# Optimization experiments

Hardware: AMD Instinct MI355X
Metric: run time of the kernel (lower is better)

The kernel has to match this reference:

```python
import jax, jax.numpy as jnp
import numpy as np

NUM_HEADS = 16


def setup_inputs() -> dict:
    key = jax.random.key(0)
    ks = jax.random.split(key, 11)
    B, S, D = 2, 8192, 1024
    scale = 1.0 / np.sqrt(D).astype(np.float32)
    return {
        "v": jax.random.normal(ks[0], (B, S, D), jnp.float32),
        "k": jax.random.normal(ks[1], (B, S, D), jnp.float32),
        "q": jax.random.normal(ks[2], (B, S, D), jnp.float32),
        "Wq": jax.random.normal(ks[3], (D, D), jnp.float32) * scale,
        "bq": jnp.zeros((D,), jnp.float32),
        "Wk": jax.random.normal(ks[4], (D, D), jnp.float32) * scale,
        "bk": jnp.zeros((D,), jnp.float32),
        "Wv": jax.random.normal(ks[5], (D, D), jnp.float32) * scale,
        "bv": jnp.zeros((D,), jnp.float32),
        "Wo": jax.random.normal(ks[6], (D, D), jnp.float32) * scale,
        "bo": jnp.zeros((D,), jnp.float32),
    }


def _mha(v, k, q, Wq, bq, Wk, bk, Wv, bv, Wo, bo):
    H = NUM_HEADS
    d_model = Wq.shape[1]
    depth = d_model // H
    # linear projections, split into heads: [B, S, H, depth]
    qh = (q @ Wq + bq).reshape(*q.shape[:-1], H, depth)
    kh = (k @ Wk + bk).reshape(*k.shape[:-1], H, depth)
    vh = (v @ Wv + bv).reshape(*v.shape[:-1], H, depth)
    # scaled dot-product attention. The original uses a chunked online-softmax
    # (memory-efficient attention, arXiv:2112.05682) which computes the exact
    # same softmax(QK^T/sqrt(d))V; we express it directly.
    scale = 1.0 / jnp.sqrt(jnp.asarray(depth, qh.dtype))
    logits = jnp.einsum('bqhd,bkhd->bhqk', qh * scale, kh,
                        precision=jax.lax.Precision.HIGHEST)
    attn = jax.nn.softmax(logits, axis=-1)
    out = jnp.einsum('bhqk,bkhd->bqhd', attn, vh,
                     precision=jax.lax.Precision.HIGHEST)
    out = out.reshape(*out.shape[:-2], d_model)
    return out @ Wo + bo


def reference(v, k, q, Wq, bq, Wk, bk, Wv, bv, Wo, bo):
    return _mha(v, k, q, Wq, bq, Wk, bk, Wv, bv, Wo, bo)
```

## Files before the change

### kernel.cpp

```cpp
#include <hip/hip_runtime.h>
#include <math.h>
#include <stdint.h>

#define H 16
#define Dm 1024
#define DH2 64
#define SLEN 8192
#define BATCH 2
#define KVBLK 64

#define WAIT_VM0 0x0F70

#if __has_builtin(__builtin_amdgcn_exp2f)
#define NEXP2(x) __builtin_amdgcn_exp2f(x)
#else
#define NEXP2(x) __builtin_exp2f(x)
#endif

typedef __attribute__((ext_vector_type(8))) short bf16x8;
typedef __attribute__((ext_vector_type(2))) float f32x2;
typedef __attribute__((ext_vector_type(4))) float f32x4;
typedef __attribute__((ext_vector_type(16))) float f32x16;
typedef __attribute__((ext_vector_type(4))) short short4v;
typedef __attribute__((ext_vector_type(4))) unsigned int uint4v;
typedef __attribute__((ext_vector_type(2))) int int2v;

#define MFMA16(a,b,c) __builtin_amdgcn_mfma_f32_16x16x32_bf16(a,b,c,0,0,0)
#define MFMA32(a,b,c) __builtin_amdgcn_mfma_f32_32x32x16_bf16(a,b,c,0,0,0)

static __device__ __forceinline__ short f2b(float f){
  unsigned u = __builtin_bit_cast(unsigned, f);
  u += 0x7fffu + ((u >> 16) & 1u);
  return (short)(u >> 16);
}

static __device__ __forceinline__ void gload16(const void* g, void* l){
  __builtin_amdgcn_global_load_lds((const __attribute__((address_space(1))) void*)g,
                                   (__attribute__((address_space(3))) void*)l, 16, 0, 0);
}

static __device__ __forceinline__ bf16x8 mkfrag_pk(const f32x2* v){
  unsigned p0, p1, p2, p3;
  asm("v_cvt_pk_bf16_f32 %0, %1, %2" : "=v"(p0) : "v"(v[0].x), "v"(v[0].y));
  asm("v_cvt_pk_bf16_f32 %0, %1, %2" : "=v"(p1) : "v"(v[1].x), "v"(v[1].y));
  asm("v_cvt_pk_bf16_f32 %0, %1, %2" : "=v"(p2) : "v"(v[2].x), "v"(v[2].y));
  asm("v_cvt_pk_bf16_f32 %0, %1, %2" : "=v"(p3) : "v"(v[3].x), "v"(v[3].y));
  uint4v u = (uint4v){p0, p1, p2, p3};
  return __builtin_bit_cast(bf16x8, u);
}

struct S8 { f32x2 v[8]; };

__global__ __launch_bounds__(256) void transpose_w_kernel(
    const float* __restrict__ Wq, const float* __restrict__ Wk,
    const float* __restrict__ Wv, const float* __restrict__ Wo,
    short* __restrict__ WqT, short* __restrict__ WkT,
    short* __restrict__ WvT, short* __restrict__ WoT)
{
  const float* W; short* WT;
  switch (blockIdx.z){
    case 0: W = Wq; WT = WqT; break;
    case 1: W = Wk; WT = WkT; break;
    case 2: W = Wv; WT = WvT; break;
    default: W = Wo; WT = WoT; break;
  }
  __shared__ float t[32][33];
  int tx = threadIdx.x & 31, ty = threadIdx.x >> 5;
  int x0 = blockIdx.x * 32, y0 = blockIdx.y * 32;
  for (int j = 0; j < 4; ++j){
    int r = ty + j * 8;
    t[r][tx] = W[(size_t)(y0 + r) * Dm + x0 + tx];
  }
  __syncthreads();
  for (int j = 0; j < 4; ++j){
    int r = ty + j * 8;
    WT[(size_t)(x0 + r) * Dm + y0 + tx] = f2b(t[tx][r]);
  }
}

__global__ __launch_bounds__(256) void proj_kernel(
    const float* __restrict__ Aq, const float* __restrict__ Ak, const float* __restrict__ Av,
    const short* __restrict__ WqT, const short* __restrict__ WkT, const short* __restrict__ WvT,
    const float* __restrict__ bq, const float* __restrict__ bk, const float* __restrict__ bv,
    short* __restrict__ Qh, short* __restrict__ Kh, short* __restrict__ VhT)
{
  const float* A; const short* WT; const float* bias;
  int z = blockIdx.z;
  if (z == 0){ A = Aq; WT = WqT; bias = bq; }
  else if (z == 1){ A = Ak; WT = WkT; bias = bk; }
  else { A = Av; WT = WvT; bias = bv; }

  __shared__ __align__(16) char smem[34816];
  short (*As)[64] = (short(*)[64])smem;
  short* Bs = (short*)(smem + 16384);

  int tid = threadIdx.x;
  int lane = tid & 63, w = tid >> 6;
  int l15 = lane & 15, lh = lane >> 4;
  int wm = w >> 1, wn = w & 1;
  int m0 = blockIdx.x * 128, n0 = blockIdx.y * 128;

  f32x4 acc[4][4];
  for (int i = 0; i < 4; ++i)
    for (int j = 0; j < 4; ++j)
      acc[i][j] = (f32x4){0.f, 0.f, 0.f, 0.f};

  for (int ko = 0; ko < 16; ++ko){
    for (int j = 0; j < 8; ++j){
      int idx = j * 256 + tid;
      int r = idx >> 4, c4 = idx & 15;
      float4 a = *(const float4*)(A + (size_t)(m0 + r) * Dm + ko * 64 + c4 * 4);
      short4v p; p[0] = f2b(a.x); p[1] = f2b(a.y); p[2] = f2b(a.z); p[3] = f2b(a.w);
      *(short4v*)&As[r][c4 * 4] = p;
    }
    for (int j = 0; j < 4; ++j){
      int c = w * 4 + j;
      int row = c * 8 + (lane >> 3), seg = lane & 7;
      gload16(WT + (size_t)(n0 + row) * Dm + ko * 64 + seg * 8, Bs + c * 512);
    }
    __builtin_amdgcn_s_waitcnt(WAIT_VM0);
    __syncthreads();
    for (int kk = 0; kk < 2; ++kk){
      bf16x8 af[4];
      for (int i = 0; i < 4; ++i)
        af[i] = *(const bf16x8*)&As[wm * 64 + i * 16 + l15][kk * 32 + lh * 8];
      for (int jj = 0; jj < 4; ++jj){
        bf16x8 bfv = *(const bf16x8*)(Bs + (size_t)(wn * 64 + jj * 16 + l15) * 64 + kk * 32 + lh * 8);
        for (int i = 0; i < 4; ++i)
          acc[i][jj] = MFMA16(af[i], bfv, acc[i][jj]);
      }
    }
    __syncthreads();
  }

  if (z < 2){
    short* out = (z == 0) ? Qh : Kh;
    float scale = (z == 0) ? 0.18033688011112042f : 1.0f;
    for (int jj = 0; jj < 4; ++jj){
      int col = n0 + wn * 64 + jj * 16 + l15;
      float bb = bias[col];
      int h = col >> 6, d = col & 63;
      for (int i = 0; i < 4; ++i)
        for (int r = 0; r < 4; ++r){
          int row = m0 + wm * 64 + i * 16 + lh * 4 + r;
          int b = row >> 13, s = row & 8191;
          out[(((size_t)b * H + h) * SLEN + s) * DH2 + d] = f2b((acc[i][jj][r] + bb) * scale);
        }
    }
  } else {
    short (*Ct)[136] = (short(*)[136])smem;
    for (int jj = 0; jj < 4; ++jj){
      int colL = wn * 64 + jj * 16 + l15;
      float bb = bias[n0 + colL];
      for (int i = 0; i < 4; ++i)
        for (int r = 0; r < 4; ++r){
          int rowL = wm * 64 + i * 16 + lh * 4 + r;
          Ct[colL][rowL] = f2b(acc[i][jj][r] + bb);
        }
    }
    __syncthreads();
    int b = m0 >> 13, s0 = m0 & 8191;
    for (int p = 0; p < 8; ++p){
      int rowC = p * 16 + (tid >> 4), seg = tid & 15;
      int4 vv = *(const int4*)&Ct[rowC][seg * 8];
      int ngl = n0 + rowC, h = ngl >> 6, d = ngl & 63;
      size_t base = (((size_t)b * H + h) * DH2 + d) * SLEN + s0;
      int sA = seg * 8;
      int b16 = sA & ~15;
      int half = (sA >> 3) & 1;
      int2v lo = (int2v){ ((int*)&vv)[0], ((int*)&vv)[1] };
      int2v hi2 = (int2v){ ((int*)&vv)[2], ((int*)&vv)[3] };
      *(int2v*)&VhT[base + b16 + half * 4]     = lo;
      *(int2v*)&VhT[base + b16 + 8 + half * 4] = hi2;
    }
  }
}

__global__ __launch_bounds__(512, 2) void attn_kernel(
    const short* __restrict__ Qh, const short* __restrict__ Kh,
    const short* __restrict__ VhT, short* __restrict__ attn_out)
{
  __shared__ __align__(16) short Ktile[2][4096];
  __shared__ __align__(16) short Vtile[2][4096];
  __shared__ float redbuf[8][32];

  const int tid = threadIdx.x;
  const int lane = tid & 63;
  const int w = tid >> 6;
  const int l31 = lane & 31;
  const int hi = lane >> 5;
  const int bh = blockIdx.y;
  const int q0 = blockIdx.x * 256 + w * 32;

  const short* Qbase = Qh + ((size_t)bh * SLEN + q0) * DH2;
  const short* Kbase = Kh + (size_t)bh * SLEN * DH2;
  const short* Vbase = VhT + (size_t)bh * DH2 * SLEN;

  bf16x8 qf[4];
#pragma unroll
  for (int ds = 0; ds < 4; ++ds)
    qf[ds] = *(const bf16x8*)(Qbase + (size_t)l31 * DH2 + ds * 16 + hi * 8);

  f32x16 Oa0, Oa1;
#pragma unroll
  for (int i = 0; i < 16; ++i){ Oa0[i] = 0.f; Oa1[i] = 0.f; }
  float l_run = 0.f;

  int koff[4];
#pragma unroll
  for (int ds = 0; ds < 4; ++ds)
    koff[ds] = l31 * 64 + (((ds * 2 + hi) ^ (l31 & 7)) * 8);
  int voff[2][4];
#pragma unroll
  for (int n = 0; n < 2; ++n)
#pragma unroll
    for (int st = 0; st < 4; ++st)
      voff[n][st] = (n * 32 + l31) * 64 + (((st * 2 + hi) ^ (l31 & 7)) * 8);

  const short* spK = Kbase + (size_t)(tid >> 3) * DH2 + (((tid & 7) ^ ((tid >> 3) & 7)) * 8);
  const short* spV = Vbase + (size_t)(tid >> 3) * SLEN + (((tid & 7) ^ ((tid >> 3) & 7)) * 8);
  short* dK0 = Ktile[0] + tid * 8; short* dK1 = Ktile[1] + tid * 8;
  short* dV0 = Vtile[0] + tid * 8; short* dV1 = Vtile[1] + tid * 8;

  gload16(spK, dK0); gload16(spV, dV0);
  spK += (size_t)KVBLK * DH2; spV += KVBLK;

  const int NT = SLEN / KVBLK;

  auto tile = [&](const short* Kt, const short* Vt, bool do_stage,
                  short* dK, short* dV){
    __builtin_amdgcn_s_waitcnt(WAIT_VM0);
    __syncthreads();
    if (do_stage){
      gload16(spK, dK);
      gload16(spV, dV);
      spK += (size_t)KVBLK * DH2; spV += KVBLK;
    }

    f32x16 sa0, sa1;
#pragma unroll
    for (int i = 0; i < 16; ++i){ sa0[i] = 0.f; sa1[i] = 0.f; }
#pragma unroll
    for (int ds = 0; ds < 4; ++ds){
      bf16x8 kf0 = *(const bf16x8*)(Kt + koff[ds]);
      bf16x8 kf1 = *(const bf16x8*)(Kt + koff[ds] + 32 * 64);
      sa0 = MFMA32(kf0, qf[ds], sa0);
      sa1 = MFMA32(kf1, qf[ds], sa1);
    }

    S8 t0 = __builtin_bit_cast(S8, sa0);
    S8 t1 = __builtin_bit_cast(S8, sa1);
#pragma unroll
    for (int i = 0; i < 8; ++i){
      t0.v[i].x = NEXP2(t0.v[i].x);
      t0.v[i].y = NEXP2(t0.v[i].y);
      t1.v[i].x = NEXP2(t1.v[i].x);
      t1.v[i].y = NEXP2(t1.v[i].y);
    }

    f32x2 s0 = ((t0.v[0] + t0.v[1]) + (t0.v[2] + t0.v[3])) +
               ((t0.v[4] + t0.v[5]) + (t0.v[6] + t0.v[7]));
    f32x2 s1 = ((t1.v[0] + t1.v[1]) + (t1.v[2] + t1.v[3])) +
               ((t1.v[4] + t1.v[5]) + (t1.v[6] + t1.v[7]));
    f32x2 st = s0 + s1;
    l_run += st.x + st.y;

    bf16x8 pa0 = mkfrag_pk(&t0.v[0]);
    bf16x8 pa1 = mkfrag_pk(&t0.v[4]);
    bf16x8 pa2 = mkfrag_pk(&t1.v[0]);
    bf16x8 pa3 = mkfrag_pk(&t1.v[4]);

    bf16x8 vb;
    vb = *(const bf16x8*)(Vt + voff[0][0]); Oa0 = MFMA32(pa0, vb, Oa0);
    vb = *(const bf16x8*)(Vt + voff[1][0]); Oa1 = MFMA32(pa0, vb, Oa1);
    vb = *(const bf16x8*)(Vt + voff[0][1]); Oa0 = MFMA32(pa1, vb, Oa0);
    vb = *(const bf16x8*)(Vt + voff[1][1]); Oa1 = MFMA32(pa1, vb, Oa1);
    vb = *(const bf16x8*)(Vt + voff[0][2]); Oa0 = MFMA32(pa2, vb, Oa0);
    vb = *(const bf16x8*)(Vt + voff[1][2]); Oa1 = MFMA32(pa2, vb, Oa1);
    vb = *(const bf16x8*)(Vt + voff[0][3]); Oa0 = MFMA32(pa3, vb, Oa0);
    vb = *(const bf16x8*)(Vt + voff[1][3]); Oa1 = MFMA32(pa3, vb, Oa1);
  };

  for (int kt = 0; kt < NT; kt += 2){
    tile(Ktile[0], Vtile[0], true,          dK1, dV1);
    tile(Ktile[1], Vtile[1], kt + 2 < NT,   dK0, dV0);
  }

  float l_tot = l_run + __shfl_xor(l_run, 32);
  float inv = 1.0f / l_tot;
  redbuf[w][l31] = inv;
  int b = bh >> 4, h = bh & 15;
#pragma unroll
  for (int j = 0; j < 4; ++j){
    f32x4 iv = *(const f32x4*)&redbuf[w][j * 8 + hi * 4];
#pragma unroll
    for (int i = 0; i < 4; ++i){
      int qi = j * 8 + hi * 4 + i;
      size_t rowoff = ((size_t)b * SLEN + q0 + qi) * Dm + h * 64;
      attn_out[rowoff + l31]      = f2b(Oa0[j * 4 + i] * iv[i]);
      attn_out[rowoff + 32 + l31] = f2b(Oa1[j * 4 + i] * iv[i]);
    }
  }
}

__global__ __launch_bounds__(256) void oproj_kernel(
    const short* __restrict__ Aattn, const short* __restrict__ WoT,
    const float* __restrict__ bo, float* __restrict__ out)
{
  __shared__ __align__(16) char smem[32768];
  short* As = (short*)smem;
  short* Bs = (short*)(smem + 16384);

  int tid = threadIdx.x;
  int lane = tid & 63, w = tid >> 6;
  int l15 = lane & 15, lh = lane >> 4;
  int wm = w >> 1, wn = w & 1;
  int m0 = blockIdx.x * 128, n0 = blockIdx.y * 128;

  f32x4 acc[4][4];
  for (int i = 0; i < 4; ++i)
    for (int j = 0; j < 4; ++j)
      acc[i][j] = (f32x4){0.f, 0.f, 0.f, 0.f};

  for (int ko = 0; ko < 16; ++ko){
    for (int j = 0; j < 4; ++j){
      int c = w * 4 + j;
      int row = c * 8 + (lane >> 3), seg = lane & 7;
      gload16(Aattn + (size_t)(m0 + row) * Dm + ko * 64 + seg * 8, As + c * 512);
      gload16(WoT   + (size_t)(n0 + row) * Dm + ko * 64 + seg * 8, Bs + c * 512);
    }
    __builtin_amdgcn_s_waitcnt(WAIT_VM0);
    __syncthreads();
    for (int kk = 0; kk < 2; ++kk){
      bf16x8 af[4];
      for (int i = 0; i < 4; ++i)
        af[i] = *(const bf16x8*)(As + (size_t)(wm * 64 + i * 16 + l15) * 64 + kk * 32 + lh * 8);
      for (int jj = 0; jj < 4; ++jj){
        bf16x8 bfv = *(const bf16x8*)(Bs + (size_t)(wn * 64 + jj * 16 + l15) * 64 + kk * 32 + lh * 8);
        for (int i = 0; i < 4; ++i)
          acc[i][jj] = MFMA16(af[i], bfv, acc[i][jj]);
      }
    }
    __syncthreads();
  }
  for (int jj = 0; jj < 4; ++jj){
    int col = n0 + wn * 64 + jj * 16 + l15;
    float bb = bo[col];
    for (int i = 0; i < 4; ++i)
      for (int r = 0; r < 4; ++r){
        int row = m0 + wm * 64 + i * 16 + lh * 4 + r;
        out[(size_t)row * Dm + col] = acc[i][jj][r] + bb;
      }
  }
}

extern "C" void kernel_launch(void* const* d_in, const int* in_sizes, int n_in,
                              void* d_out, int out_size, void* d_ws, size_t ws_size,
                              hipStream_t stream)
{
  const float* v  = (const float*)d_in[0];
  const float* k  = (const float*)d_in[1];
  const float* q  = (const float*)d_in[2];
  const float* Wq = (const float*)d_in[3];
  const float* bq = (const float*)d_in[4];
  const float* Wk = (const float*)d_in[5];
  const float* bk = (const float*)d_in[6];
  const float* Wv = (const float*)d_in[7];
  const float* bv = (const float*)d_in[8];
  const float* Wo = (const float*)d_in[9];
  const float* bo = (const float*)d_in[10];
  float* out = (float*)d_out;

  char* ws = (char*)d_ws;
  const size_t MB = 1u << 20;
  short* WqT = (short*)(ws + 0 * MB);
  short* WkT = (short*)(ws + 2 * MB);
  short* WvT = (short*)(ws + 4 * MB);
  short* WoT = (short*)(ws + 6 * MB);
  short* Qh  = (short*)(ws + 8 * MB);
  short* Kh  = (short*)(ws + 40 * MB);
  short* VhT = (short*)(ws + 72 * MB);
  short* Ao  = (short*)(ws + 104 * MB);

  transpose_w_kernel<<<dim3(32, 32, 4), 256, 0, stream>>>(Wq, Wk, Wv, Wo, WqT, WkT, WvT, WoT);
  proj_kernel<<<dim3(128, 8, 3), 256, 0, stream>>>(q, k, v, WqT, WkT, WvT, bq, bk, bv, Qh, Kh, VhT);
  attn_kernel<<<dim3(32, 32), 512, 0, stream>>>(Qh, Kh, VhT, Ao);
  oproj_kernel<<<dim3(128, 8), 256, 0, stream>>>(Ao, WoT, bo, out);
}
```

Before: 829.3 us.

## Precast activations to bf16 and double attention KV tile size

Adds a separate kernel that casts the q/k/v activations to bf16 once, so each projection block can stage A tiles with direct global-to-LDS loads instead of re-reading fp32 and converting per n-block. Separately, the attention KV block grows from 64 to 128 keys, with each tile processed as two 64-key halves, halving the number of barrier/stage iterations. The precast path costs extra workspace and an extra full pass over the inputs, and the larger LDS footprint may cut attention occupancy.

```diff
diff --git a/kernel.cpp b/kernel.cpp
--- a/kernel.cpp
+++ b/kernel.cpp
@@ -7,7 +7,7 @@
 #define DH2 64
 #define SLEN 8192
 #define BATCH 2
-#define KVBLK 64
+#define KVBLK 128
 
 #define WAIT_VM0 0x0F70
 
@@ -51,6 +51,30 @@
 
 struct S8 { f32x2 v[8]; };
 
+__global__ __launch_bounds__(256) void cast_a_kernel(
+    const float* __restrict__ q, const float* __restrict__ k, const float* __restrict__ v,
+    short* __restrict__ Aq, short* __restrict__ Ak, short* __restrict__ Av)
+{
+  const float* src; short* dst;
+  switch (blockIdx.y){
+    case 0: src = q; dst = Aq; break;
+    case 1: src = k; dst = Ak; break;
+    default: src = v; dst = Av; break;
+  }
+  const size_t n = (size_t)BATCH * SLEN * Dm;
+  size_t i0 = ((size_t)blockIdx.x * 256 + threadIdx.x) * 8;
+  size_t stride = (size_t)gridDim.x * 256 * 8;
+  for (size_t i = i0; i < n; i += stride){
+    float4 a = *(const float4*)(src + i);
+    float4 b = *(const float4*)(src + i + 4);
+    short4v p, r;
+    p[0] = f2b(a.x); p[1] = f2b(a.y); p[2] = f2b(a.z); p[3] = f2b(a.w);
+    r[0] = f2b(b.x); r[1] = f2b(b.y); r[2] = f2b(b.z); r[3] = f2b(b.w);
+    *(short4v*)(dst + i) = p;
+    *(short4v*)(dst + i + 4) = r;
+  }
+}
+
 __global__ __launch_bounds__(256) void transpose_w_kernel(
     const float* __restrict__ Wq, const float* __restrict__ Wk,
     const float* __restrict__ Wv, const float* __restrict__ Wo,
@@ -78,20 +102,23 @@
   }
 }
 
+template<bool PRECAST>
 __global__ __launch_bounds__(256) void proj_kernel(
-    const float* __restrict__ Aq, const float* __restrict__ Ak, const float* __restrict__ Av,
+    const float* __restrict__ Afq, const float* __restrict__ Afk, const float* __restrict__ Afv,
+    const short* __restrict__ Abq, const short* __restrict__ Abk, const short* __restrict__ Abv,
     const short* __restrict__ WqT, const short* __restrict__ WkT, const short* __restrict__ WvT,
     const float* __restrict__ bq, const float* __restrict__ bk, const float* __restrict__ bv,
     short* __restrict__ Qh, short* __restrict__ Kh, short* __restrict__ VhT)
 {
-  const float* A; const short* WT; const float* bias;
+  const float* Af; const short* Ab; const short* WT; const float* bias;
   int z = blockIdx.z;
-  if (z == 0){ A = Aq; WT = WqT; bias = bq; }
-  else if (z == 1){ A = Ak; WT = WkT; bias = bk; }
-  else { A = Av; WT = WvT; bias = bv; }
+  if (z == 0){ Af = Afq; Ab = Abq; WT = WqT; bias = bq; }
+  else if (z == 1){ Af = Afk; Ab = Abk; WT = WkT; bias = bk; }
+  else { Af = Afv; Ab = Abv; WT = WvT; bias = bv; }
 
   __shared__ __align__(16) char smem[34816];
   short (*As)[64] = (short(*)[64])smem;
+  short* Asl = (short*)smem;
   short* Bs = (short*)(smem + 16384);
 
   int tid = threadIdx.x;
@@ -106,12 +133,20 @@
       acc[i][j] = (f32x4){0.f, 0.f, 0.f, 0.f};
 
   for (int ko = 0; ko < 16; ++ko){
-    for (int j = 0; j < 8; ++j){
-      int idx = j * 256 + tid;
-      int r = idx >> 4, c4 = idx & 15;
-      float4 a = *(const float4*)(A + (size_t)(m0 + r) * Dm + ko * 64 + c4 * 4);
-      short4v p; p[0] = f2b(a.x); p[1] = f2b(a.y); p[2] = f2b(a.z); p[3] = f2b(a.w);
-      *(short4v*)&As[r][c4 * 4] = p;
+    if (PRECAST){
+      for (int j = 0; j < 4; ++j){
+        int c = w * 4 + j;
+        int row = c * 8 + (lane >> 3), seg = lane & 7;
+        gload16(Ab + (size_t)(m0 + row) * Dm + ko * 64 + seg * 8, Asl + c * 512);
+      }
+    } else {
+      for (int j = 0; j < 8; ++j){
+        int idx = j * 256 + tid;
+        int r = idx >> 4, c4 = idx & 15;
+        float4 a = *(const float4*)(Af + (size_t)(m0 + r) * Dm + ko * 64 + c4 * 4);
+        short4v p; p[0] = f2b(a.x); p[1] = f2b(a.y); p[2] = f2b(a.z); p[3] = f2b(a.w);
+        *(short4v*)&As[r][c4 * 4] = p;
+      }
     }
     for (int j = 0; j < 4; ++j){
       int c = w * 4 + j;
@@ -149,6 +184,7 @@
     }
   } else {
     short (*Ct)[136] = (short(*)[136])smem;
+    __syncthreads();
     for (int jj = 0; jj < 4; ++jj){
       int colL = wn * 64 + jj * 16 + l15;
       float bb = bias[n0 + colL];
@@ -180,8 +216,8 @@
     const short* __restrict__ Qh, const short* __restrict__ Kh,
     const short* __restrict__ VhT, short* __restrict__ attn_out)
 {
-  __shared__ __align__(16) short Ktile[2][4096];
-  __shared__ __align__(16) short Vtile[2][4096];
+  __shared__ __align__(16) short Ktile[2][8192];
+  __shared__ __align__(16) short Vtile[2][8192];
   __shared__ float redbuf[8][32];
 
   const int tid = threadIdx.x;
@@ -201,9 +237,9 @@
   for (int ds = 0; ds < 4; ++ds)
     qf[ds] = *(const bf16x8*)(Qbase + (size_t)l31 * DH2 + ds * 16 + hi * 8);
 
-  f32x16 Oa0, Oa1;
-#pragma unroll
-  for (int i = 0; i < 16; ++i){ Oa0[i] = 0.f; Oa1[i] = 0.f; }
+  f32x16 Oa0, Oa1, Zacc;
+#pragma unroll
+  for (int i = 0; i < 16; ++i){ Oa0[i] = 0.f; Oa1[i] = 0.f; Zacc[i] = 0.f; }
   float l_run = 0.f;
 
   int koff[4];
@@ -215,14 +251,16 @@
   for (int n = 0; n < 2; ++n)
 #pragma unroll
     for (int st = 0; st < 4; ++st)
-      voff[n][st] = (n * 32 + l31) * 64 + (((st * 2 + hi) ^ (l31 & 7)) * 8);
+      voff[n][st] = (n * 32 + l31) * 128 + (((st * 2 + hi) ^ (l31 & 7)) * 8);
 
   const short* spK = Kbase + (size_t)(tid >> 3) * DH2 + (((tid & 7) ^ ((tid >> 3) & 7)) * 8);
-  const short* spV = Vbase + (size_t)(tid >> 3) * SLEN + (((tid & 7) ^ ((tid >> 3) & 7)) * 8);
+  const int vkc = tid & 15, vh = vkc >> 3, vc8 = vkc & 7, vd = tid >> 4;
+  const short* spV = Vbase + (size_t)vd * SLEN + vh * 64 + ((vc8 ^ (vd & 7)) * 8);
   short* dK0 = Ktile[0] + tid * 8; short* dK1 = Ktile[1] + tid * 8;
   short* dV0 = Vtile[0] + tid * 8; short* dV1 = Vtile[1] + tid * 8;
 
-  gload16(spK, dK0); gload16(spV, dV0);
+  gload16(spK, dK0); gload16(spK + 64 * DH2, dK0 + 4096);
+  gload16(spV, dV0); gload16(spV + (size_t)32 * SLEN, dV0 + 4096);
   spK += (size_t)KVBLK * DH2; spV += KVBLK;
 
   const int NT = SLEN / KVBLK;
@@ -232,58 +270,65 @@
     __builtin_amdgcn_s_waitcnt(WAIT_VM0);
     __syncthreads();
     if (do_stage){
-      gload16(spK, dK);
-      gload16(spV, dV);
+      gload16(spK, dK); gload16(spK + 64 * DH2, dK + 4096);
+      gload16(spV, dV); gload16(spV + (size_t)32 * SLEN, dV + 4096);
       spK += (size_t)KVBLK * DH2; spV += KVBLK;
     }
 
-    f32x16 sa0, sa1;
-#pragma unroll
-    for (int i = 0; i < 16; ++i){ sa0[i] = 0.f; sa1[i] = 0.f; }
-#pragma unroll
-    for (int ds = 0; ds < 4; ++ds){
-      bf16x8 kf0 = *(const bf16x8*)(Kt + koff[ds]);
-      bf16x8 kf1 = *(const bf16x8*)(Kt + koff[ds] + 32 * 64);
-      sa0 = MFMA32(kf0, qf[ds], sa0);
-      sa1 = MFMA32(kf1, qf[ds], sa1);
-    }
-
-    S8 t0 = __builtin_bit_cast(S8, sa0);
-    S8 t1 = __builtin_bit_cast(S8, sa1);
-#pragma unroll
-    for (int i = 0; i < 8; ++i){
-      t0.v[i].x = NEXP2(t0.v[i].x);
-      t0.v[i].y = NEXP2(t0.v[i].y);
-      t1.v[i].x = NEXP2(t1.v[i].x);
-      t1.v[i].y = NEXP2(t1.v[i].y);
-    }
-
-    f32x2 s0 = ((t0.v[0] + t0.v[1]) + (t0.v[2] + t0.v[3])) +
-               ((t0.v[4] + t0.v[5]) + (t0.v[6] + t0.v[7]));
-    f32x2 s1 = ((t1.v[0] + t1.v[1]) + (t1.v[2] + t1.v[3])) +
-               ((t1.v[4] + t1.v[5]) + (t1.v[6] + t1.v[7]));
-    f32x2 st = s0 + s1;
-    l_run += st.x + st.y;
-
-    bf16x8 pa0 = mkfrag_pk(&t0.v[0]);
-    bf16x8 pa1 = mkfrag_pk(&t0.v[4]);
-    bf16x8 pa2 = mkfrag_pk(&t1.v[0]);
-    bf16x8 pa3 = mkfrag_pk(&t1.v[4]);
-
-    bf16x8 vb;
-    vb = *(const bf16x8*)(Vt + voff[0][0]); Oa0 = MFMA32(pa0, vb, Oa0);
-    vb = *(const bf16x8*)(Vt + voff[1][0]); Oa1 = MFMA32(pa0, vb, Oa1);
-    vb = *(const bf16x8*)(Vt + voff[0][1]); Oa0 = MFMA32(pa1, vb, Oa0);
-    vb = *(const bf16x8*)(Vt + voff[1][1]); Oa1 = MFMA32(pa1, vb, Oa1);
-    vb = *(const bf16x8*)(Vt + voff[0][2]); Oa0 = MFMA32(pa2, vb, Oa0);
-    vb = *(const bf16x8*)(Vt + voff[1][2]); Oa1 = MFMA32(pa2, vb, Oa1);
-    vb = *(const bf16x8*)(Vt + voff[0][3]); Oa0 = MFMA32(pa3, vb, Oa0);
-    vb = *(const bf16x8*)(Vt + voff[1][3]); Oa1 = MFMA32(pa3, vb, Oa1);
+#pragma unroll
+    for (int half = 0; half < 2; ++half){
+      const short* Kh_ = Kt + half * 4096;
+      const short* Vh_ = Vt + half * 64;
+
+      bf16x8 kf0 = *(const bf16x8*)(Kh_ + koff[0]);
+      bf16x8 kf1 = *(const bf16x8*)(Kh_ + koff[0] + 2048);
+      f32x16 sa0 = MFMA32(kf0, qf[0], Zacc);
+      f32x16 sa1 = MFMA32(kf1, qf[0], Zacc);
+#pragma unroll
+      for (int ds = 1; ds < 4; ++ds){
+        kf0 = *(const bf16x8*)(Kh_ + koff[ds]);
+        kf1 = *(const bf16x8*)(Kh_ + koff[ds] + 2048);
+        sa0 = MFMA32(kf0, qf[ds], sa0);
+        sa1 = MFMA32(kf1, qf[ds], sa1);
+      }
+
+      S8 t0 = __builtin_bit_cast(S8, sa0);
+      S8 t1 = __builtin_bit_cast(S8, sa1);
+#pragma unroll
+      for (int i = 0; i < 8; ++i){
+        t0.v[i].x = NEXP2(t0.v[i].x);
+        t0.v[i].y = NEXP2(t0.v[i].y);
+        t1.v[i].x = NEXP2(t1.v[i].x);
+        t1.v[i].y = NEXP2(t1.v[i].y);
+      }
+
+      f32x2 s0 = ((t0.v[0] + t0.v[1]) + (t0.v[2] + t0.v[3])) +
+                 ((t0.v[4] + t0.v[5]) + (t0.v[6] + t0.v[7]));
+      f32x2 s1 = ((t1.v[0] + t1.v[1]) + (t1.v[2] + t1.v[3])) +
+                 ((t1.v[4] + t1.v[5]) + (t1.v[6] + t1.v[7]));
+      f32x2 st = s0 + s1;
+      l_run += st.x + st.y;
+
+      bf16x8 pa0 = mkfrag_pk(&t0.v[0]);
+      bf16x8 pa1 = mkfrag_pk(&t0.v[4]);
+      bf16x8 pa2 = mkfrag_pk(&t1.v[0]);
+      bf16x8 pa3 = mkfrag_pk(&t1.v[4]);
+
+      bf16x8 vb;
+      vb = *(const bf16x8*)(Vh_ + voff[0][0]); Oa0 = MFMA32(pa0, vb, Oa0);
+      vb = *(const bf16x8*)(Vh_ + voff[1][0]); Oa1 = MFMA32(pa0, vb, Oa1);
+      vb = *(const bf16x8*)(Vh_ + voff[0][1]); Oa0 = MFMA32(pa1, vb, Oa0);
+      vb = *(const bf16x8*)(Vh_ + voff[1][1]); Oa1 = MFMA32(pa1, vb, Oa1);
+      vb = *(const bf16x8*)(Vh_ + voff[0][2]); Oa0 = MFMA32(pa2, vb, Oa0);
+      vb = *(const bf16x8*)(Vh_ + voff[1][2]); Oa1 = MFMA32(pa2, vb, Oa1);
+      vb = *(const bf16x8*)(Vh_ + voff[0][3]); Oa0 = MFMA32(pa3, vb, Oa0);
+      vb = *(const bf16x8*)(Vh_ + voff[1][3]); Oa1 = MFMA32(pa3, vb, Oa1);
+    }
   };
 
   for (int kt = 0; kt < NT; kt += 2){
-    tile(Ktile[0], Vtile[0], true,          dK1, dV1);
-    tile(Ktile[1], Vtile[1], kt + 2 < NT,   dK0, dV0);
+    tile(Ktile[0], Vtile[0], true,         dK1, dV1);
+    tile(Ktile[1], Vtile[1], kt + 2 < NT,  dK0, dV0);
   }
 
   float l_tot = l_run + __shfl_xor(l_run, 32);
@@ -381,9 +426,21 @@
   short* Kh  = (short*)(ws + 40 * MB);
   short* VhT = (short*)(ws + 72 * MB);
   short* Ao  = (short*)(ws + 104 * MB);
+  short* Aqb = (short*)(ws + 136 * MB);
+  short* Akb = (short*)(ws + 168 * MB);
+  short* Avb = (short*)(ws + 200 * MB);
+
+  bool precast = ws_size >= (size_t)232 * MB;
 
   transpose_w_kernel<<<dim3(32, 32, 4), 256, 0, stream>>>(Wq, Wk, Wv, Wo, WqT, WkT, WvT, WoT);
-  proj_kernel<<<dim3(128, 8, 3), 256, 0, stream>>>(q, k, v, WqT, WkT, WvT, bq, bk, bv, Qh, Kh, VhT);
+  if (precast){
+    cast_a_kernel<<<dim3(2048, 3), 256, 0, stream>>>(q, k, v, Aqb, Akb, Avb);
+    proj_kernel<true><<<dim3(128, 8, 3), 256, 0, stream>>>(
+        q, k, v, Aqb, Akb, Avb, WqT, WkT, WvT, bq, bk, bv, Qh, Kh, VhT);
+  } else {
+    proj_kernel<false><<<dim3(128, 8, 3), 256, 0, stream>>>(
+        q, k, v, Aqb, Akb, Avb, WqT, WkT, WvT, bq, bk, bv, Qh, Kh, VhT);
+  }
   attn_kernel<<<dim3(32, 32), 512, 0, stream>>>(Qh, Kh, VhT, Ao);
   oproj_kernel<<<dim3(128, 8), 256, 0, stream>>>(Ao, WoT, bo, out);
 }
```

After: 864.5 us. 4.2% more time.
